# Kernel optimization log

Measured on AMD Instinct MI355X. Metric: run time of the kernel, lower is better.

Reference implementation:

```python
import jax, jax.numpy as jnp
import numpy as np

N = 1_000_000   # posts
D = 256         # embedding dim
T = 5           # trait labels
U = 16384       # users (all ids assumed present; see notes)


def setup_inputs() -> dict:
    key = jax.random.key(0)
    k1, k2, k3 = jax.random.split(key, 3)
    z = jax.random.normal(k1, (N, D), dtype=jnp.float32)
    user_ids = jax.random.randint(k2, (N,), 0, U, dtype=jnp.int64)
    y = jax.random.uniform(k3, (N, T), dtype=jnp.float32)
    return {"z": z, "user_ids": user_ids, "y": y}


def reference(z, user_ids, y):
    # group-by-user mean of z and thresholded mean of y, users sorted by id
    seg = user_ids.astype(jnp.int32)
    counts = jax.ops.segment_sum(jnp.ones((seg.shape[0],), z.dtype), seg, num_segments=U)
    denom = jnp.maximum(counts, 1.0)[:, None]          # [U, 1]
    agg_z = jax.ops.segment_sum(z, seg, num_segments=U) / denom   # [U, D]
    mean_y = jax.ops.segment_sum(y, seg, num_segments=U) / denom  # [U, T]
    agg_y = (mean_y >= 0.5).astype(z.dtype)
    return agg_z, agg_y
```

## Files before the change

### kernel.cpp

```cpp
#include <hip/hip_runtime.h>

#define NPOSTS 1000000
#define DIM    256
#define TLAB   5
#define NUSERS 16384
#define SLOTS  192

typedef float vfloat4 __attribute__((ext_vector_type(4)));

__global__ void scatter4_kernel(const int4* __restrict__ ids4,
                                int* __restrict__ cursor,
                                int* __restrict__ sorted, int n4) {
    const int i = blockIdx.x * blockDim.x + threadIdx.x;
    if (i < n4) {
        const int4 v = ids4[i];
        const int b = i * 4;
        sorted[v.x * SLOTS + atomicAdd(&cursor[v.x], 1)] = b;
        sorted[v.y * SLOTS + atomicAdd(&cursor[v.y], 1)] = b + 1;
        sorted[v.z * SLOTS + atomicAdd(&cursor[v.z], 1)] = b + 2;
        sorted[v.w * SLOTS + atomicAdd(&cursor[v.w], 1)] = b + 3;
    }
}

__global__ __launch_bounds__(256) void agg_kernel(const float* __restrict__ z,
                                                  const float* __restrict__ y,
                                                  const int* __restrict__ sorted,
                                                  const int* __restrict__ cursor,
                                                  float* __restrict__ out_z,
                                                  float* __restrict__ out_y) {
    const int u    = blockIdx.x;
    const int t    = threadIdx.x;
    const int w    = __builtin_amdgcn_readfirstlane(t >> 6);
    const int lane = t & 63;
    const int c      = cursor[u];
    const int padded = (c + 15) & ~15;
    const int q      = padded >> 2;

    const int* sp = sorted + u * SLOTS + w * q;
    const size_t col = (size_t)(lane * 4);

    vfloat4 acc = (vfloat4){0.f, 0.f, 0.f, 0.f};
    float  yacc = 0.f;

    for (int k = 0; k < q; k += 4) {
        const int i0 = sp[k + 0];
        const int i1 = sp[k + 1];
        const int i2 = sp[k + 2];
        const int i3 = sp[k + 3];
        const vfloat4 v0 = __builtin_nontemporal_load(
            reinterpret_cast<const vfloat4*>(z + (size_t)i0 * DIM + col));
        const vfloat4 v1 = __builtin_nontemporal_load(
            reinterpret_cast<const vfloat4*>(z + (size_t)i1 * DIM + col));
        const vfloat4 v2 = __builtin_nontemporal_load(
            reinterpret_cast<const vfloat4*>(z + (size_t)i2 * DIM + col));
        const vfloat4 v3 = __builtin_nontemporal_load(
            reinterpret_cast<const vfloat4*>(z + (size_t)i3 * DIM + col));
        if (lane < TLAB) {
            yacc += y[(size_t)i0 * TLAB + lane] + y[(size_t)i1 * TLAB + lane]
                  + y[(size_t)i2 * TLAB + lane] + y[(size_t)i3 * TLAB + lane];
        }
        acc += (v0 + v1) + (v2 + v3);
    }

    __shared__ float shz[4][DIM];
    __shared__ float shy[4][TLAB];
    *reinterpret_cast<vfloat4*>(&shz[w][col]) = acc;
    if (lane < TLAB) shy[w][lane] = yacc;
    __syncthreads();

    const int   pads  = padded - c;
    const float fpads = (float)pads;
    const float denom = (c > 0) ? (float)c : 1.0f;
    float s = (shz[0][t] + shz[1][t]) + (shz[2][t] + shz[3][t]);
    s -= fpads * z[t];
    __builtin_nontemporal_store(s / denom, &out_z[(size_t)u * DIM + t]);
    if (t < TLAB) {
        float ys = (shy[0][t] + shy[1][t]) + (shy[2][t] + shy[3][t]);
        ys -= fpads * y[t];
        __builtin_nontemporal_store(((ys / denom) >= 0.5f) ? 1.0f : 0.0f,
                                    &out_y[(size_t)u * TLAB + t]);
    }
}

extern "C" void kernel_launch(void* const* d_in, const int* in_sizes, int n_in,
                              void* d_out, int out_size, void* d_ws, size_t ws_size,
                              hipStream_t stream) {
    const float* z   = (const float*)d_in[0];
    const int*   ids = (const int*)d_in[1];
    const float* y   = (const float*)d_in[2];

    const int n = in_sizes[1];

    int* sorted = (int*)d_ws;
    int* cursor = sorted + (size_t)NUSERS * SLOTS;

    float* out_z = (float*)d_out;
    float* out_y = out_z + (size_t)NUSERS * DIM;

    (void)hipMemsetAsync(sorted, 0,
                   ((size_t)NUSERS * SLOTS + NUSERS) * sizeof(int), stream);

    const int n4 = n / 4;
    scatter4_kernel<<<(n4 + 255) / 256, 256, 0, stream>>>(
        (const int4*)ids, cursor, sorted, n4);

    agg_kernel<<<NUSERS, 256, 0, stream>>>(z, y, sorted, cursor, out_z, out_y);
}
```

Baseline: 245.6 us.

## Fuse y accumulation into scatter via atomics and shrink workspace memset

Moves the per-user sum of y labels into the scatter kernel using float atomicAdd, removing the scattered y gathers from the aggregation kernel. The large memset of the sorted index buffer is dropped; instead, padded slots are masked to index 0 in the agg loop so the existing pad correction stays valid. This trades a big memset and strided y reads for about 5 atomics per post and extra compares in the gather loop. Float atomics make the y sums order-nondeterministic.

```diff
diff --git a/kernel.cpp b/kernel.cpp
--- a/kernel.cpp
+++ b/kernel.cpp
@@ -7,25 +7,44 @@
 #define SLOTS  192
 
 typedef float vfloat4 __attribute__((ext_vector_type(4)));
+typedef int   vint4   __attribute__((ext_vector_type(4)));
 
-__global__ void scatter4_kernel(const int4* __restrict__ ids4,
+__global__ void scatter4_kernel(const vint4* __restrict__ ids4,
+                                const float* __restrict__ y,
                                 int* __restrict__ cursor,
-                                int* __restrict__ sorted, int n4) {
+                                int* __restrict__ sorted,
+                                float* __restrict__ yacc, int n4) {
     const int i = blockIdx.x * blockDim.x + threadIdx.x;
-    if (i < n4) {
-        const int4 v = ids4[i];
-        const int b = i * 4;
-        sorted[v.x * SLOTS + atomicAdd(&cursor[v.x], 1)] = b;
-        sorted[v.y * SLOTS + atomicAdd(&cursor[v.y], 1)] = b + 1;
-        sorted[v.z * SLOTS + atomicAdd(&cursor[v.z], 1)] = b + 2;
-        sorted[v.w * SLOTS + atomicAdd(&cursor[v.w], 1)] = b + 3;
+    if (i >= n4) return;
+    const vint4 v = __builtin_nontemporal_load(&ids4[i]);
+    const int b = i * 4;
+
+    const float* yp = y + (size_t)b * TLAB;
+    float yv[4 * TLAB];
+#pragma unroll
+    for (int j = 0; j < TLAB; ++j) {
+        const vfloat4 t = __builtin_nontemporal_load(
+            reinterpret_cast<const vfloat4*>(yp + 4 * j));
+        yv[4 * j + 0] = t.x; yv[4 * j + 1] = t.y;
+        yv[4 * j + 2] = t.z; yv[4 * j + 3] = t.w;
+    }
+
+    const int us[4] = {v.x, v.y, v.z, v.w};
+#pragma unroll
+    for (int j = 0; j < 4; ++j) {
+        const int u = us[j];
+        const int pos = atomicAdd(&cursor[u], 1);
+        sorted[u * SLOTS + pos] = b + j;
+#pragma unroll
+        for (int tr = 0; tr < TLAB; ++tr)
+            atomicAdd(&yacc[u * TLAB + tr], yv[j * TLAB + tr]);
     }
 }
 
 __global__ __launch_bounds__(256) void agg_kernel(const float* __restrict__ z,
-                                                  const float* __restrict__ y,
                                                   const int* __restrict__ sorted,
                                                   const int* __restrict__ cursor,
+                                                  const float* __restrict__ yacc,
                                                   float* __restrict__ out_z,
                                                   float* __restrict__ out_y) {
     const int u    = blockIdx.x;
@@ -37,16 +56,16 @@
     const int q      = padded >> 2;
 
     const int* sp = sorted + u * SLOTS + w * q;
+    const int  pos0 = w * q;
     const size_t col = (size_t)(lane * 4);
 
     vfloat4 acc = (vfloat4){0.f, 0.f, 0.f, 0.f};
-    float  yacc = 0.f;
 
     for (int k = 0; k < q; k += 4) {
-        const int i0 = sp[k + 0];
-        const int i1 = sp[k + 1];
-        const int i2 = sp[k + 2];
-        const int i3 = sp[k + 3];
+        const int i0 = (pos0 + k + 0 < c) ? sp[k + 0] : 0;
+        const int i1 = (pos0 + k + 1 < c) ? sp[k + 1] : 0;
+        const int i2 = (pos0 + k + 2 < c) ? sp[k + 2] : 0;
+        const int i3 = (pos0 + k + 3 < c) ? sp[k + 3] : 0;
         const vfloat4 v0 = __builtin_nontemporal_load(
             reinterpret_cast<const vfloat4*>(z + (size_t)i0 * DIM + col));
         const vfloat4 v1 = __builtin_nontemporal_load(
@@ -55,29 +74,21 @@
             reinterpret_cast<const vfloat4*>(z + (size_t)i2 * DIM + col));
         const vfloat4 v3 = __builtin_nontemporal_load(
             reinterpret_cast<const vfloat4*>(z + (size_t)i3 * DIM + col));
-        if (lane < TLAB) {
-            yacc += y[(size_t)i0 * TLAB + lane] + y[(size_t)i1 * TLAB + lane]
-                  + y[(size_t)i2 * TLAB + lane] + y[(size_t)i3 * TLAB + lane];
-        }
         acc += (v0 + v1) + (v2 + v3);
     }
 
     __shared__ float shz[4][DIM];
-    __shared__ float shy[4][TLAB];
     *reinterpret_cast<vfloat4*>(&shz[w][col]) = acc;
-    if (lane < TLAB) shy[w][lane] = yacc;
     __syncthreads();
 
-    const int   pads  = padded - c;
-    const float fpads = (float)pads;
+    const float fpads = (float)(padded - c);
     const float denom = (c > 0) ? (float)c : 1.0f;
     float s = (shz[0][t] + shz[1][t]) + (shz[2][t] + shz[3][t]);
     s -= fpads * z[t];
     __builtin_nontemporal_store(s / denom, &out_z[(size_t)u * DIM + t]);
     if (t < TLAB) {
-        float ys = (shy[0][t] + shy[1][t]) + (shy[2][t] + shy[3][t]);
-        ys -= fpads * y[t];
-        __builtin_nontemporal_store(((ys / denom) >= 0.5f) ? 1.0f : 0.0f,
+        const float mean_y = yacc[u * TLAB + t] / denom;
+        __builtin_nontemporal_store((mean_y >= 0.5f) ? 1.0f : 0.0f,
                                     &out_y[(size_t)u * TLAB + t]);
     }
 }
@@ -91,18 +102,20 @@
 
     const int n = in_sizes[1];
 
-    int* sorted = (int*)d_ws;
-    int* cursor = sorted + (size_t)NUSERS * SLOTS;
+    int*   sorted = (int*)d_ws;
+    int*   cursor = sorted + (size_t)NUSERS * SLOTS;
+    float* yacc   = (float*)(cursor + NUSERS);
 
     float* out_z = (float*)d_out;
     float* out_y = out_z + (size_t)NUSERS * DIM;
 
-    (void)hipMemsetAsync(sorted, 0,
-                   ((size_t)NUSERS * SLOTS + NUSERS) * sizeof(int), stream);
+    (void)hipMemsetAsync(cursor, 0,
+                         (size_t)NUSERS * (1 + TLAB) * sizeof(int), stream);
 
     const int n4 = n / 4;
     scatter4_kernel<<<(n4 + 255) / 256, 256, 0, stream>>>(
-        (const int4*)ids, cursor, sorted, n4);
+        (const vint4*)ids, y, cursor, sorted, yacc, n4);
 
-    agg_kernel<<<NUSERS, 256, 0, stream>>>(z, y, sorted, cursor, out_z, out_y);
+    agg_kernel<<<NUSERS, 256, 0, stream>>>(z, sorted, cursor, yacc,
+                                           out_z, out_y);
 }
```

Measured after the change: 475.5 us. 1.94x slower.
